# Kernel optimization log

Measured on AMD Instinct MI355X. Metric: run time of the kernel, lower is better.

## Reference

```python
import jax, jax.numpy as jnp
import numpy as np

DIM = 1024
NUM_HEADS = 16
HEAD_DIM = DIM // NUM_HEADS
B, L = 4, 4096


def setup_inputs() -> dict:
    key = jax.random.key(0)
    ks = jax.random.split(key, 11)
    s = 1.0 / np.sqrt(DIM)
    inp = {
        'q_seq': jax.random.normal(ks[0], (B, L, DIM), jnp.float32),
        'k_seq': jax.random.normal(ks[1], (B, L, DIM), jnp.float32),
        'v_seq': jax.random.normal(ks[2], (B, L, DIM), jnp.float32),
        'Wq': jax.random.normal(ks[3], (DIM, DIM), jnp.float32) * s,
        'bq': jax.random.normal(ks[4], (DIM,), jnp.float32) * s,
        'Wk': jax.random.normal(ks[5], (DIM, DIM), jnp.float32) * s,
        'bk': jax.random.normal(ks[6], (DIM,), jnp.float32) * s,
        'Wv': jax.random.normal(ks[7], (DIM, DIM), jnp.float32) * s,
        'bv': jax.random.normal(ks[8], (DIM,), jnp.float32) * s,
        'Wo': jax.random.normal(ks[9], (DIM, DIM), jnp.float32) * s,
        'bo': jax.random.normal(ks[10], (DIM,), jnp.float32) * s,
        'extract_common': 1,
    }
    return inp


def _heads(x):
    # [B, L, DIM] -> [B, H, L, D]
    Bb, Ll, _ = x.shape
    return x.reshape(Bb, Ll, NUM_HEADS, HEAD_DIM).transpose(0, 2, 1, 3)


def reference(q_seq, k_seq, v_seq, Wq, bq, Wk, bk, Wv, bv, Wo, bo, extract_common):
    Q = _heads(q_seq @ Wq.T + bq)   # [B, H, Lq, D]
    K = _heads(k_seq @ Wk.T + bk)   # [B, H, Lk, D]
    V = _heads(v_seq @ Wv.T + bv)   # [B, H, Lv, D]
    # softmax over the sequence dimension of K (torch dim=2 of [B,H,L,D])
    K_probs = jax.nn.softmax(K, axis=2)
    # context = K_probs^T @ V : [B, H, D, D]
    context = jnp.einsum('bhld,bhle->bhde', K_probs, V)
    attended = jnp.einsum('bhld,bhde->bhle', Q, context)  # [B, H, Lq, D]
    if extract_common:
        target = attended
    else:
        target = V - attended
    Bb, _, Ll, _ = target.shape
    target = target.transpose(0, 2, 1, 3).reshape(Bb, Ll, DIM)
    return target @ Wo.T + bo
```

## Files before the change

kernel.cpp:

```cpp
#include <hip/hip_runtime.h>
#include <cmath>

typedef __bf16 bf16x8 __attribute__((ext_vector_type(8)));
typedef float f32x4 __attribute__((ext_vector_type(4)));
typedef unsigned short us8 __attribute__((ext_vector_type(8)));

__device__ __forceinline__ unsigned short f2bf(float f) {
    union { float f; unsigned u; } x; x.f = f;
    unsigned u = x.u + 0x7FFFu + ((x.u >> 16) & 1u);
    return (unsigned short)(u >> 16);
}
__device__ __forceinline__ float bf2f(unsigned short h) {
    union { unsigned u; float f; } x; x.u = ((unsigned)h) << 16;
    return x.f;
}

__device__ __forceinline__ us8 cvt8(const float* p) {
    f32x4 a = *(const f32x4*)p;
    f32x4 b = *(const f32x4*)(p + 4);
    union { bf16x8 h; us8 u; } cv;
    cv.h[0] = (__bf16)a[0]; cv.h[1] = (__bf16)a[1];
    cv.h[2] = (__bf16)a[2]; cv.h[3] = (__bf16)a[3];
    cv.h[4] = (__bf16)b[0]; cv.h[5] = (__bf16)b[1];
    cv.h[6] = (__bf16)b[2]; cv.h[7] = (__bf16)b[3];
    return cv.u;
}

__device__ __forceinline__ void gl2lds16(const unsigned short* g, unsigned short* l) {
    __builtin_amdgcn_global_load_lds(
        (const __attribute__((address_space(1))) unsigned int*)g,
        (__attribute__((address_space(3))) unsigned int*)l, 16, 0, 0);
}

__global__ __launch_bounds__(256)
void cvt_kernel(const float* __restrict__ src, unsigned short* __restrict__ dst) {
    const size_t i = ((size_t)blockIdx.x * 256 + threadIdx.x) * 8;
    *(us8*)(dst + i) = cvt8(src + i);
}

__global__ __launch_bounds__(256)
void cvt_w4(const float* __restrict__ s0, const float* __restrict__ s1,
            const float* __restrict__ s2, const float* __restrict__ s3,
            unsigned short* __restrict__ d0, unsigned short* __restrict__ d1,
            unsigned short* __restrict__ d2, unsigned short* __restrict__ d3) {
    const float* sp[4] = {s0, s1, s2, s3};
    unsigned short* dp[4] = {d0, d1, d2, d3};
    const float* src = sp[blockIdx.y];
    unsigned short* dst = dp[blockIdx.y];
    const size_t i = ((size_t)blockIdx.x * 256 + threadIdx.x) * 8;
    *(us8*)(dst + i) = cvt8(src + i);
}

__device__ __forceinline__ void swz_tiles(int& m0, int& n0) {
    const int slot = blockIdx.x + (blockIdx.y << 3);
    const int w = ((slot & 7) << 7) | (slot >> 3);
    m0 = (w >> 3) << 7;
    n0 = (w & 7) << 7;
}

template<int MODE, bool BF>
__global__ __launch_bounds__(256)
void gemm_proj(const void* __restrict__ Ap, const void* __restrict__ Wp,
               const float* __restrict__ bias,
               unsigned short* __restrict__ outT,
               float* __restrict__ S)
{
    __shared__ __align__(16) unsigned short lds[17408];

    const int tid = threadIdx.x;
    const int wid = tid >> 6, lane = tid & 63;
    const int quad = lane >> 4, l16 = lane & 15;
    const int waveM = wid >> 1, waveN = wid & 1;
    int m0, n0; swz_tiles(m0, n0);
    const int srow = tid >> 2;
    const int scol = (tid & 3) * 8;
    const int r4 = lane >> 2, c8 = (lane & 3) * 8;

    f32x4 acc[4][4] = {};

    if (BF) {
        const unsigned short* A = (const unsigned short*)Ap;
        const unsigned short* W = (const unsigned short*)Wp;
        for (int s = wid; s < 8; s += 4) {
            const int row = s * 16 + r4;
            gl2lds16(A + (size_t)(m0 + row) * 1024 + c8, lds + s * 512);
            gl2lds16(W + (size_t)(n0 + row) * 1024 + c8, lds + 4096 + s * 512);
        }
    } else {
        const float* A = (const float*)Ap;
        const float* W = (const float*)Wp;
#pragma unroll
        for (int p = 0; p < 2; ++p) {
            const int row = p * 64 + srow;
            *(us8*)(lds + row * 32 + scol) = cvt8(A + (size_t)(m0 + row) * 1024 + scol);
            *(us8*)(lds + 4096 + row * 32 + scol) = cvt8(W + (size_t)(n0 + row) * 1024 + scol);
        }
    }
    __syncthreads();

    int cur = 0;
    for (int k0 = 0; k0 < 1024; k0 += 32) {
        const int nxt = cur ^ 1;
        if (k0 < 992) {
            if (BF) {
                const unsigned short* A = (const unsigned short*)Ap;
                const unsigned short* W = (const unsigned short*)Wp;
                for (int s = wid; s < 8; s += 4) {
                    const int row = s * 16 + r4;
                    gl2lds16(A + (size_t)(m0 + row) * 1024 + k0 + 32 + c8,
                             lds + nxt * 8192 + s * 512);
                    gl2lds16(W + (size_t)(n0 + row) * 1024 + k0 + 32 + c8,
                             lds + nxt * 8192 + 4096 + s * 512);
                }
            } else {
                const float* A = (const float*)Ap;
                const float* W = (const float*)Wp;
#pragma unroll
                for (int p = 0; p < 2; ++p) {
                    const int row = p * 64 + srow;
                    *(us8*)(lds + nxt * 8192 + row * 32 + scol) =
                        cvt8(A + (size_t)(m0 + row) * 1024 + k0 + 32 + scol);
                    *(us8*)(lds + nxt * 8192 + 4096 + row * 32 + scol) =
                        cvt8(W + (size_t)(n0 + row) * 1024 + k0 + 32 + scol);
                }
            }
        }
        const unsigned short* ldsA = lds + cur * 8192;
        const unsigned short* ldsB = ldsA + 4096;
        bf16x8 af[4], bfr[4];
#pragma unroll
        for (int i = 0; i < 4; ++i)
            af[i] = *(const bf16x8*)(ldsA + (waveM * 64 + i * 16 + l16) * 32 + quad * 8);
#pragma unroll
        for (int j = 0; j < 4; ++j)
            bfr[j] = *(const bf16x8*)(ldsB + (waveN * 64 + j * 16 + l16) * 32 + quad * 8);
#pragma unroll
        for (int i = 0; i < 4; ++i)
#pragma unroll
            for (int j = 0; j < 4; ++j)
                acc[i][j] = __builtin_amdgcn_mfma_f32_16x16x32_bf16(af[i], bfr[j], acc[i][j], 0, 0, 0);
        __syncthreads();
        cur = nxt;
    }

    const int b = m0 >> 12, l0 = m0 & 4095;
#pragma unroll
    for (int j = 0; j < 4; ++j) {
        const int nn = waveN * 64 + j * 16 + l16;
        const float bc = bias[n0 + nn];
        float ssum = 0.f;
#pragma unroll
        for (int i = 0; i < 4; ++i)
#pragma unroll
            for (int r = 0; r < 4; ++r) {
                const int mm = waveM * 64 + i * 16 + quad * 4 + r;
                float v = acc[i][j][r] + bc;
                if (MODE == 1) v = expf(fminf(fmaxf(v, -30.f), 30.f));
                lds[nn * 136 + mm] = f2bf(v);
                ssum += v;
            }
        if (MODE == 1) {
            ssum += __shfl_xor(ssum, 16);
            ssum += __shfl_xor(ssum, 32);
            if (lane < 16)
                atomicAdd(&S[(size_t)b * 1024 + n0 + waveN * 64 + j * 16 + lane], ssum);
        }
    }
    __syncthreads();
    const int seg = (tid & 15) * 8;
#pragma unroll
    for (int it = 0; it < 8; ++it) {
        const int nn = (tid >> 4) + it * 16;
        us8 v = *(const us8*)&lds[nn * 136 + seg];
        *(us8*)(outT + ((size_t)b * 1024 + n0 + nn) * 4096 + l0 + seg) = v;
    }
}

__global__ __launch_bounds__(256)
void ctx_kernel(const unsigned short* __restrict__ Vt,
                const unsigned short* __restrict__ Et,
                float* __restrict__ ctxf)
{
    __shared__ __align__(16) unsigned short lds[8192];

    const int tid = threadIdx.x;
    const int wid = tid >> 6, lane = tid & 63;
    const int quad = lane >> 4, l16 = lane & 15;
    const int b = blockIdx.z, h = blockIdx.y;
    const int lbase = blockIdx.x * 512;

    const unsigned short* Arow = Vt + ((size_t)b * 1024 + h * 64) * 4096;
    const unsigned short* Brow = Et + ((size_t)b * 1024 + h * 64) * 4096;

    const int srow = tid >> 2;
    const int scol = (tid & 3) * 8;

    f32x4 acc[4] = {};

    {
        us8 va = *(const us8*)(Arow + (size_t)srow * 4096 + lbase + scol);
        us8 vb = *(const us8*)(Brow + (size_t)srow * 4096 + lbase + scol);
        *(us8*)(lds + srow * 32 + scol) = va;
        *(us8*)(lds + 2048 + srow * 32 + scol) = vb;
    }
    __syncthreads();

    int cur = 0;
    for (int k0 = 0; k0 < 512; k0 += 32) {
        const int nxt = cur ^ 1;
        us8 na = {}, nb = {};
        const bool pf = (k0 < 480);
        if (pf) {
            na = *(const us8*)(Arow + (size_t)srow * 4096 + lbase + k0 + 32 + scol);
            nb = *(const us8*)(Brow + (size_t)srow * 4096 + lbase + k0 + 32 + scol);
        }
        const unsigned short* ldsA = lds + cur * 4096;
        const unsigned short* ldsB = ldsA + 2048;
        bf16x8 a = *(const bf16x8*)(ldsA + (wid * 16 + l16) * 32 + quad * 8);
#pragma unroll
        for (int j = 0; j < 4; ++j) {
            bf16x8 bb = *(const bf16x8*)(ldsB + (j * 16 + l16) * 32 + quad * 8);
            acc[j] = __builtin_amdgcn_mfma_f32_16x16x32_bf16(a, bb, acc[j], 0, 0, 0);
        }
        if (pf) {
            *(us8*)(lds + nxt * 4096 + srow * 32 + scol) = na;
            *(us8*)(lds + nxt * 4096 + 2048 + srow * 32 + scol) = nb;
        }
        __syncthreads();
        cur = nxt;
    }
    float* base = ctxf + ((size_t)(b * 16 + h)) * 4096;
#pragma unroll
    for (int j = 0; j < 4; ++j)
#pragma unroll
        for (int r = 0; r < 4; ++r) {
            const int e = wid * 16 + quad * 4 + r;
            const int d = j * 16 + l16;
            atomicAdd(base + e * 64 + d, acc[j][r]);
        }
}

__global__ __launch_bounds__(256)
void ctx_norm(const float* __restrict__ ctxf, const float* __restrict__ S,
              unsigned short* __restrict__ ctxb)
{
    const int i = blockIdx.x * 256 + threadIdx.x;
    const int d = i & 63;
    const int bh = i >> 12;
    const int b = bh >> 4, h = bh & 15;
    ctxb[i] = f2bf(ctxf[i] / S[b * 1024 + h * 64 + d]);
}

template<bool BF>
__global__ __launch_bounds__(256)
void gemm_qattn(const void* __restrict__ Ap, const void* __restrict__ Wp,
                const float* __restrict__ bias,
                const unsigned short* __restrict__ ctxb,
                const unsigned short* __restrict__ Vt,
                const int* __restrict__ ec,
                unsigned short* __restrict__ att)
{
    __shared__ __align__(16) unsigned short lds[26624];
    unsigned short* ldsQ = lds;
    unsigned short* ldsC = lds + 17408;

    const int tid = threadIdx.x;
    const int wid = tid >> 6, lane = tid & 63;
    const int quad = lane >> 4, l16 = lane & 15;
    const int waveM = wid >> 1, waveN = wid & 1;
    int m0, n0; swz_tiles(m0, n0);
    const int b = m0 >> 12;
    const int srow = tid >> 2, scol = (tid & 3) * 8;
    const int r4 = lane >> 2, c8 = (lane & 3) * 8;

    {
        const int e2 = tid >> 1;
        const int sg = (tid & 1) * 32;
        const unsigned short* src = ctxb +
            (((size_t)(b * 16) + (n0 >> 6) + (e2 >> 6)) * 64 + (e2 & 63)) * 64 + sg;
#pragma unroll
        for (int u = 0; u < 4; ++u)
            *(us8*)&ldsC[e2 * 72 + sg + u * 8] = *(const us8*)(src + u * 8);
    }

    f32x4 acc[4][4] = {};

    if (BF) {
        const unsigned short* A = (const unsigned short*)Ap;
        const unsigned short* W = (const unsigned short*)Wp;
        for (int s = wid; s < 8; s += 4) {
            const int row = s * 16 + r4;
            gl2lds16(A + (size_t)(m0 + row) * 1024 + c8, lds + s * 512);
            gl2lds16(W + (size_t)(n0 + row) * 1024 + c8, lds + 4096 + s * 512);
        }
    } else {
        const float* A = (const float*)Ap;
        const float* W = (const float*)Wp;
#pragma unroll
        for (int p = 0; p < 2; ++p) {
            const int row = p * 64 + srow;
            *(us8*)(lds + row * 32 + scol) = cvt8(A + (size_t)(m0 + row) * 1024 + scol);
            *(us8*)(lds + 4096 + row * 32 + scol) = cvt8(W + (size_t)(n0 + row) * 1024 + scol);
        }
    }
    __syncthreads();

    int cur = 0;
    for (int k0 = 0; k0 < 1024; k0 += 32) {
        const int nxt = cur ^ 1;
        if (k0 < 992) {
            if (BF) {
                const unsigned short* A = (const unsigned short*)Ap;
                const unsigned short* W = (const unsigned short*)Wp;
                for (int s = wid; s < 8; s += 4) {
                    const int row = s * 16 + r4;
                    gl2lds16(A + (size_t)(m0 + row) * 1024 + k0 + 32 + c8,
                             lds + nxt * 8192 + s * 512);
                    gl2lds16(W + (size_t)(n0 + row) * 1024 + k0 + 32 + c8,
                             lds + nxt * 8192 + 4096 + s * 512);
                }
            } else {
                const float* A = (const float*)Ap;
                const float* W = (const float*)Wp;
#pragma unroll
                for (int p = 0; p < 2; ++p) {
                    const int row = p * 64 + srow;
                    *(us8*)(lds + nxt * 8192 + row * 32 + scol) =
                        cvt8(A + (size_t)(m0 + row) * 1024 + k0 + 32 + scol);
                    *(us8*)(lds + nxt * 8192 + 4096 + row * 32 + scol) =
                        cvt8(W + (size_t)(n0 + row) * 1024 + k0 + 32 + scol);
                }
            }
        }
        const unsigned short* ldsA = lds + cur * 8192;
        const unsigned short* ldsB = ldsA + 4096;
        bf16x8 af[4], bfr[4];
#pragma unroll
        for (int i = 0; i < 4; ++i)
            af[i] = *(const bf16x8*)(ldsA + (waveM * 64 + i * 16 + l16) * 32 + quad * 8);
#pragma unroll
        for (int j = 0; j < 4; ++j)
            bfr[j] = *(const bf16x8*)(ldsB + (waveN * 64 + j * 16 + l16) * 32 + quad * 8);
#pragma unroll
        for (int i = 0; i < 4; ++i)
#pragma unroll
            for (int j = 0; j < 4; ++j)
                acc[i][j] = __builtin_amdgcn_mfma_f32_16x16x32_bf16(af[i], bfr[j], acc[i][j], 0, 0, 0);
        __syncthreads();
        cur = nxt;
    }

#pragma unroll
    for (int j = 0; j < 4; ++j) {
        const int nn = waveN * 64 + j * 16 + l16;
        const float bc = bias[n0 + nn];
#pragma unroll
        for (int i = 0; i < 4; ++i)
#pragma unroll
            for (int r = 0; r < 4; ++r) {
                const int mm = waveM * 64 + i * 16 + quad * 4 + r;
                ldsQ[mm * 136 + nn] = f2bf(acc[i][j][r] + bc);
            }
    }
    __syncthreads();

    f32x4 acc2[4][4] = {};
#pragma unroll
    for (int ks = 0; ks < 64; ks += 32) {
        bf16x8 aq[4], cq[4];
#pragma unroll
        for (int i = 0; i < 4; ++i)
            aq[i] = *(const bf16x8*)&ldsQ[(waveM * 64 + i * 16 + l16) * 136 + waveN * 64 + ks + quad * 8];
#pragma unroll
        for (int j = 0; j < 4; ++j)
            cq[j] = *(const bf16x8*)&ldsC[(waveN * 64 + j * 16 + l16) * 72 + ks + quad * 8];
#pragma unroll
        for (int i = 0; i < 4; ++i)
#pragma unroll
            for (int j = 0; j < 4; ++j)
                acc2[i][j] = __builtin_amdgcn_mfma_f32_16x16x32_bf16(aq[i], cq[j], acc2[i][j], 0, 0, 0);
    }

    const int common = ec[0];
#pragma unroll
    for (int i = 0; i < 4; ++i)
#pragma unroll
        for (int j = 0; j < 4; ++j)
#pragma unroll
            for (int r = 0; r < 4; ++r) {
                const int lrow = m0 + waveM * 64 + i * 16 + quad * 4 + r;
                const int chan = n0 + waveN * 64 + j * 16 + l16;
                float vv = acc2[i][j][r];
                if (!common)
                    vv = bf2f(Vt[((size_t)(lrow >> 12) * 1024 + chan) * 4096 + (lrow & 4095)]) - vv;
                att[(size_t)lrow * 1024 + chan] = f2bf(vv);
            }
}

template<bool BF>
__global__ __launch_bounds__(256)
void gemm_out(const unsigned short* __restrict__ A, const void* __restrict__ Wp,
              const float* __restrict__ bias,
              float* __restrict__ outP)
{
    __shared__ __align__(16) unsigned short lds[16384];

    const int tid = threadIdx.x;
    const int wid = tid >> 6, lane = tid & 63;
    const int quad = lane >> 4, l16 = lane & 15;
    const int waveM = wid >> 1, waveN = wid & 1;
    int m0, n0; swz_tiles(m0, n0);
    const int srow = tid >> 2, scol = (tid & 3) * 8;
    const int r4 = lane >> 2, c8 = (lane & 3) * 8;

    f32x4 acc[4][4] = {};

    if (BF) {
        const unsigned short* W = (const unsigned short*)Wp;
        for (int s = wid; s < 8; s += 4) {
            const int row = s * 16 + r4;
            gl2lds16(A + (size_t)(m0 + row) * 1024 + c8, lds + s * 512);
            gl2lds16(W + (size_t)(n0 + row) * 1024 + c8, lds + 4096 + s * 512);
        }
    } else {
        const float* W = (const float*)Wp;
#pragma unroll
        for (int p = 0; p < 2; ++p) {
            const int row = p * 64 + srow;
            *(us8*)(lds + row * 32 + scol) = *(const us8*)(A + (size_t)(m0 + row) * 1024 + scol);
            *(us8*)(lds + 4096 + row * 32 + scol) = cvt8(W + (size_t)(n0 + row) * 1024 + scol);
        }
    }
    __syncthreads();

    int cur = 0;
    for (int k0 = 0; k0 < 1024; k0 += 32) {
        const int nxt = cur ^ 1;
        if (k0 < 992) {
            if (BF) {
                const unsigned short* W = (const unsigned short*)Wp;
                for (int s = wid; s < 8; s += 4) {
                    const int row = s * 16 + r4;
                    gl2lds16(A + (size_t)(m0 + row) * 1024 + k0 + 32 + c8,
                             lds + nxt * 8192 + s * 512);
                    gl2lds16(W + (size_t)(n0 + row) * 1024 + k0 + 32 + c8,
                             lds + nxt * 8192 + 4096 + s * 512);
                }
            } else {
                const float* W = (const float*)Wp;
#pragma unroll
                for (int p = 0; p < 2; ++p) {
                    const int row = p * 64 + srow;
                    *(us8*)(lds + nxt * 8192 + row * 32 + scol) =
                        *(const us8*)(A + (size_t)(m0 + row) * 1024 + k0 + 32 + scol);
                    *(us8*)(lds + nxt * 8192 + 4096 + row * 32 + scol) =
                        cvt8(W + (size_t)(n0 + row) * 1024 + k0 + 32 + scol);
                }
            }
        }
        const unsigned short* ldsA = lds + cur * 8192;
        const unsigned short* ldsB = ldsA + 4096;
        bf16x8 af[4], bfr[4];
#pragma unroll
        for (int i = 0; i < 4; ++i)
            af[i] = *(const bf16x8*)(ldsA + (waveM * 64 + i * 16 + l16) * 32 + quad * 8);
#pragma unroll
        for (int j = 0; j < 4; ++j)
            bfr[j] = *(const bf16x8*)(ldsB + (waveN * 64 + j * 16 + l16) * 32 + quad * 8);
#pragma unroll
        for (int i = 0; i < 4; ++i)
#pragma unroll
            for (int j = 0; j < 4; ++j)
                acc[i][j] = __builtin_amdgcn_mfma_f32_16x16x32_bf16(af[i], bfr[j], acc[i][j], 0, 0, 0);
        __syncthreads();
        cur = nxt;
    }

#pragma unroll
    for (int j = 0; j < 4; ++j) {
        const int col = n0 + waveN * 64 + j * 16 + l16;
        const float bc = bias[col];
#pragma unroll
        for (int i = 0; i < 4; ++i)
#pragma unroll
            for (int r = 0; r < 4; ++r) {
                const int row = m0 + waveM * 64 + i * 16 + quad * 4 + r;
                outP[(size_t)row * 1024 + col] = acc[i][j][r] + bc;
            }
    }
}

extern "C" void kernel_launch(void* const* d_in, const int* in_sizes, int n_in,
                              void* d_out, int out_size, void* d_ws, size_t ws_size,
                              hipStream_t stream)
{
    const float* q  = (const float*)d_in[0];
    const float* k  = (const float*)d_in[1];
    const float* v  = (const float*)d_in[2];
    const float* Wq = (const float*)d_in[3];
    const float* bq = (const float*)d_in[4];
    const float* Wk = (const float*)d_in[5];
    const float* bk = (const float*)d_in[6];
    const float* Wv = (const float*)d_in[7];
    const float* bv = (const float*)d_in[8];
    const float* Wo = (const float*)d_in[9];
    const float* bo = (const float*)d_in[10];
    const int* ec   = (const int*)d_in[11];

    char* ws = (char*)d_ws;
    const size_t NEED_FAST = 110641152;
    const dim3 gblk(8, 128, 1);
    const dim3 gctx(8, 16, 4);

    if (ws_size >= NEED_FAST) {
        unsigned short* Ab   = (unsigned short*)(ws);
        unsigned short* Et   = (unsigned short*)(ws + 33554432);
        unsigned short* Vt   = (unsigned short*)(ws + 67108864);
        unsigned short* Wkb  = (unsigned short*)(ws + 100663296);
        unsigned short* Wvb  = (unsigned short*)(ws + 102760448);
        unsigned short* Wqb  = (unsigned short*)(ws + 104857600);
        unsigned short* Wob  = (unsigned short*)(ws + 106954752);
        float*          ctxf = (float*)(ws + 109051904);
        float*          S    = (float*)(ws + 110100480);
        unsigned short* ctxb = (unsigned short*)(ws + 110116864);
        unsigned short* att  = Et;

        hipMemsetAsync(S, 0, 4096 * sizeof(float), stream);
        hipMemsetAsync(ctxf, 0, 4 * 16 * 64 * 64 * sizeof(float), stream);

        cvt_w4<<<dim3(512, 4), 256, 0, stream>>>(Wk, Wv, Wq, Wo, Wkb, Wvb, Wqb, Wob);

        cvt_kernel<<<8192, 256, 0, stream>>>(k, Ab);
        gemm_proj<1, true><<<gblk, 256, 0, stream>>>(Ab, Wkb, bk, Et, S);

        cvt_kernel<<<8192, 256, 0, stream>>>(v, Ab);
        gemm_proj<2, true><<<gblk, 256, 0, stream>>>(Ab, Wvb, bv, Vt, nullptr);

        ctx_kernel<<<gctx, 256, 0, stream>>>(Vt, Et, ctxf);
        ctx_norm<<<1024, 256, 0, stream>>>(ctxf, S, ctxb);

        cvt_kernel<<<8192, 256, 0, stream>>>(q, Ab);
        gemm_qattn<true><<<gblk, 256, 0, stream>>>(Ab, Wqb, bq, ctxb, Vt, ec, att);

        gemm_out<true><<<gblk, 256, 0, stream>>>(att, Wob, bo, (float*)d_out);
    } else {
        unsigned short* Et   = (unsigned short*)(ws);
        unsigned short* Vt   = (unsigned short*)(ws + 33554432);
        float*          ctxf = (float*)(ws + 67108864);
        float*          S    = (float*)(ws + 68157440);
        unsigned short* ctxb = (unsigned short*)(ws + 68173824);
        unsigned short* att  = Et;

        hipMemsetAsync(S, 0, 4096 * sizeof(float), stream);
        hipMemsetAsync(ctxf, 0, 4 * 16 * 64 * 64 * sizeof(float), stream);

        gemm_proj<1, false><<<gblk, 256, 0, stream>>>(k, Wk, bk, Et, S);
        gemm_proj<2, false><<<gblk, 256, 0, stream>>>(v, Wv, bv, Vt, nullptr);
        ctx_kernel<<<gctx, 256, 0, stream>>>(Vt, Et, ctxf);
        ctx_norm<<<1024, 256, 0, stream>>>(ctxf, S, ctxb);
        gemm_qattn<false><<<gblk, 256, 0, stream>>>(q, Wq, bq, ctxb, Vt, ec, att);
        gemm_out<false><<<gblk, 256, 0, stream>>>(att, Wo, bo, (float*)d_out);
    }
}
```

Measured before the change: 458.3 us.

## Fuse activation fp32-to-bf16 conversion and context normalization into GEMM kernels

Drops the three standalone cvt_kernel passes over q/k/v and the ctx_norm kernel. The projection GEMMs now read fp32 activations directly. They prefetch the next K tile into registers before the MFMAs and pack to bf16 into LDS after them. The qattn kernel divides ctxf by S while loading its context tile. This removes a full write and re-read of three 32MB bf16 buffers plus several launches. In exchange, the GEMMs read twice the activation bytes per tile and hold more registers, and the async LDS load path for A is lost.

```diff
diff --git a/kernel.cpp b/kernel.cpp
--- a/kernel.cpp
+++ b/kernel.cpp
@@ -15,9 +15,7 @@
     return x.f;
 }
 
-__device__ __forceinline__ us8 cvt8(const float* p) {
-    f32x4 a = *(const f32x4*)p;
-    f32x4 b = *(const f32x4*)(p + 4);
+__device__ __forceinline__ us8 pack8(f32x4 a, f32x4 b) {
     union { bf16x8 h; us8 u; } cv;
     cv.h[0] = (__bf16)a[0]; cv.h[1] = (__bf16)a[1];
     cv.h[2] = (__bf16)a[2]; cv.h[3] = (__bf16)a[3];
@@ -26,16 +24,16 @@
     return cv.u;
 }
 
+__device__ __forceinline__ us8 cvt8(const float* p) {
+    f32x4 a = *(const f32x4*)p;
+    f32x4 b = *(const f32x4*)(p + 4);
+    return pack8(a, b);
+}
+
 __device__ __forceinline__ void gl2lds16(const unsigned short* g, unsigned short* l) {
     __builtin_amdgcn_global_load_lds(
         (const __attribute__((address_space(1))) unsigned int*)g,
         (__attribute__((address_space(3))) unsigned int*)l, 16, 0, 0);
-}
-
-__global__ __launch_bounds__(256)
-void cvt_kernel(const float* __restrict__ src, unsigned short* __restrict__ dst) {
-    const size_t i = ((size_t)blockIdx.x * 256 + threadIdx.x) * 8;
-    *(us8*)(dst + i) = cvt8(src + i);
 }
 
 __global__ __launch_bounds__(256)
@@ -58,9 +56,9 @@
     n0 = (w & 7) << 7;
 }
 
-template<int MODE, bool BF>
+template<int MODE, bool WBF>
 __global__ __launch_bounds__(256)
-void gemm_proj(const void* __restrict__ Ap, const void* __restrict__ Wp,
+void gemm_proj(const float* __restrict__ A, const void* __restrict__ Wp,
                const float* __restrict__ bias,
                unsigned short* __restrict__ outT,
                float* __restrict__ S)
@@ -72,56 +70,52 @@
     const int quad = lane >> 4, l16 = lane & 15;
     const int waveM = wid >> 1, waveN = wid & 1;
     int m0, n0; swz_tiles(m0, n0);
-    const int srow = tid >> 2;
-    const int scol = (tid & 3) * 8;
+    const int srow = tid >> 2, scol = (tid & 3) * 8;
     const int r4 = lane >> 2, c8 = (lane & 3) * 8;
 
     f32x4 acc[4][4] = {};
 
-    if (BF) {
-        const unsigned short* A = (const unsigned short*)Ap;
+    if (WBF) {
         const unsigned short* W = (const unsigned short*)Wp;
-        for (int s = wid; s < 8; s += 4) {
-            const int row = s * 16 + r4;
-            gl2lds16(A + (size_t)(m0 + row) * 1024 + c8, lds + s * 512);
-            gl2lds16(W + (size_t)(n0 + row) * 1024 + c8, lds + 4096 + s * 512);
-        }
+        for (int s = wid; s < 8; s += 4)
+            gl2lds16(W + (size_t)(n0 + s * 16 + r4) * 1024 + c8, lds + 4096 + s * 512);
     } else {
-        const float* A = (const float*)Ap;
         const float* W = (const float*)Wp;
 #pragma unroll
-        for (int p = 0; p < 2; ++p) {
-            const int row = p * 64 + srow;
-            *(us8*)(lds + row * 32 + scol) = cvt8(A + (size_t)(m0 + row) * 1024 + scol);
-            *(us8*)(lds + 4096 + row * 32 + scol) = cvt8(W + (size_t)(n0 + row) * 1024 + scol);
-        }
-    }
+        for (int p = 0; p < 2; ++p)
+            *(us8*)(lds + 4096 + (p * 64 + srow) * 32 + scol) =
+                cvt8(W + (size_t)(n0 + p * 64 + srow) * 1024 + scol);
+    }
+#pragma unroll
+    for (int p = 0; p < 2; ++p)
+        *(us8*)(lds + (p * 64 + srow) * 32 + scol) =
+            cvt8(A + (size_t)(m0 + p * 64 + srow) * 1024 + scol);
     __syncthreads();
 
     int cur = 0;
     for (int k0 = 0; k0 < 1024; k0 += 32) {
         const int nxt = cur ^ 1;
-        if (k0 < 992) {
-            if (BF) {
-                const unsigned short* A = (const unsigned short*)Ap;
+        const bool pf = (k0 < 992);
+        f32x4 pa[2][2], pw[2][2];
+        if (pf) {
+#pragma unroll
+            for (int p = 0; p < 2; ++p) {
+                const float* src = A + (size_t)(m0 + p * 64 + srow) * 1024 + k0 + 32 + scol;
+                pa[p][0] = *(const f32x4*)src;
+                pa[p][1] = *(const f32x4*)(src + 4);
+            }
+            if (WBF) {
                 const unsigned short* W = (const unsigned short*)Wp;
-                for (int s = wid; s < 8; s += 4) {
-                    const int row = s * 16 + r4;
-                    gl2lds16(A + (size_t)(m0 + row) * 1024 + k0 + 32 + c8,
-                             lds + nxt * 8192 + s * 512);
-                    gl2lds16(W + (size_t)(n0 + row) * 1024 + k0 + 32 + c8,
+                for (int s = wid; s < 8; s += 4)
+                    gl2lds16(W + (size_t)(n0 + s * 16 + r4) * 1024 + k0 + 32 + c8,
                              lds + nxt * 8192 + 4096 + s * 512);
-                }
             } else {
-                const float* A = (const float*)Ap;
                 const float* W = (const float*)Wp;
 #pragma unroll
                 for (int p = 0; p < 2; ++p) {
-                    const int row = p * 64 + srow;
-                    *(us8*)(lds + nxt * 8192 + row * 32 + scol) =
-                        cvt8(A + (size_t)(m0 + row) * 1024 + k0 + 32 + scol);
-                    *(us8*)(lds + nxt * 8192 + 4096 + row * 32 + scol) =
-                        cvt8(W + (size_t)(n0 + row) * 1024 + k0 + 32 + scol);
+                    const float* srcw = W + (size_t)(n0 + p * 64 + srow) * 1024 + k0 + 32 + scol;
+                    pw[p][0] = *(const f32x4*)srcw;
+                    pw[p][1] = *(const f32x4*)(srcw + 4);
                 }
             }
         }
@@ -139,6 +133,16 @@
 #pragma unroll
             for (int j = 0; j < 4; ++j)
                 acc[i][j] = __builtin_amdgcn_mfma_f32_16x16x32_bf16(af[i], bfr[j], acc[i][j], 0, 0, 0);
+        if (pf) {
+#pragma unroll
+            for (int p = 0; p < 2; ++p)
+                *(us8*)(lds + nxt * 8192 + (p * 64 + srow) * 32 + scol) = pack8(pa[p][0], pa[p][1]);
+            if (!WBF) {
+#pragma unroll
+                for (int p = 0; p < 2; ++p)
+                    *(us8*)(lds + nxt * 8192 + 4096 + (p * 64 + srow) * 32 + scol) = pack8(pw[p][0], pw[p][1]);
+            }
+        }
         __syncthreads();
         cur = nxt;
     }
@@ -240,22 +244,12 @@
         }
 }
 
+template<bool WBF>
 __global__ __launch_bounds__(256)
-void ctx_norm(const float* __restrict__ ctxf, const float* __restrict__ S,
-              unsigned short* __restrict__ ctxb)
-{
-    const int i = blockIdx.x * 256 + threadIdx.x;
-    const int d = i & 63;
-    const int bh = i >> 12;
-    const int b = bh >> 4, h = bh & 15;
-    ctxb[i] = f2bf(ctxf[i] / S[b * 1024 + h * 64 + d]);
-}
-
-template<bool BF>
-__global__ __launch_bounds__(256)
-void gemm_qattn(const void* __restrict__ Ap, const void* __restrict__ Wp,
+void gemm_qattn(const float* __restrict__ A, const void* __restrict__ Wp,
                 const float* __restrict__ bias,
-                const unsigned short* __restrict__ ctxb,
+                const float* __restrict__ ctxf,
+                const float* __restrict__ Sv,
                 const unsigned short* __restrict__ Vt,
                 const int* __restrict__ ec,
                 unsigned short* __restrict__ att)
@@ -276,59 +270,65 @@
     {
         const int e2 = tid >> 1;
         const int sg = (tid & 1) * 32;
-        const unsigned short* src = ctxb +
-            (((size_t)(b * 16) + (n0 >> 6) + (e2 >> 6)) * 64 + (e2 & 63)) * 64 + sg;
-#pragma unroll
-        for (int u = 0; u < 4; ++u)
-            *(us8*)&ldsC[e2 * 72 + sg + u * 8] = *(const us8*)(src + u * 8);
+        const int hh = (n0 >> 6) + (e2 >> 6);
+        const float* srcf = ctxf + (((size_t)(b * 16) + hh) * 64 + (e2 & 63)) * 64 + sg;
+        const float* Sp = Sv + (size_t)b * 1024 + hh * 64 + sg;
+#pragma unroll
+        for (int u = 0; u < 4; ++u) {
+            f32x4 c0 = *(const f32x4*)(srcf + u * 8);
+            f32x4 c1 = *(const f32x4*)(srcf + u * 8 + 4);
+            union { bf16x8 h; us8 uu; } cv;
+#pragma unroll
+            for (int j = 0; j < 4; ++j) cv.h[j] = (__bf16)(c0[j] / Sp[u * 8 + j]);
+#pragma unroll
+            for (int j = 0; j < 4; ++j) cv.h[4 + j] = (__bf16)(c1[j] / Sp[u * 8 + 4 + j]);
+            *(us8*)&ldsC[e2 * 72 + sg + u * 8] = cv.uu;
+        }
     }
 
     f32x4 acc[4][4] = {};
 
-    if (BF) {
-        const unsigned short* A = (const unsigned short*)Ap;
+    if (WBF) {
         const unsigned short* W = (const unsigned short*)Wp;
-        for (int s = wid; s < 8; s += 4) {
-            const int row = s * 16 + r4;
-            gl2lds16(A + (size_t)(m0 + row) * 1024 + c8, lds + s * 512);
-            gl2lds16(W + (size_t)(n0 + row) * 1024 + c8, lds + 4096 + s * 512);
-        }
+        for (int s = wid; s < 8; s += 4)
+            gl2lds16(W + (size_t)(n0 + s * 16 + r4) * 1024 + c8, lds + 4096 + s * 512);
     } else {
-        const float* A = (const float*)Ap;
         const float* W = (const float*)Wp;
 #pragma unroll
-        for (int p = 0; p < 2; ++p) {
-            const int row = p * 64 + srow;
-            *(us8*)(lds + row * 32 + scol) = cvt8(A + (size_t)(m0 + row) * 1024 + scol);
-            *(us8*)(lds + 4096 + row * 32 + scol) = cvt8(W + (size_t)(n0 + row) * 1024 + scol);
-        }
-    }
+        for (int p = 0; p < 2; ++p)
+            *(us8*)(lds + 4096 + (p * 64 + srow) * 32 + scol) =
+                cvt8(W + (size_t)(n0 + p * 64 + srow) * 1024 + scol);
+    }
+#pragma unroll
+    for (int p = 0; p < 2; ++p)
+        *(us8*)(lds + (p * 64 + srow) * 32 + scol) =
+            cvt8(A + (size_t)(m0 + p * 64 + srow) * 1024 + scol);
     __syncthreads();
 
     int cur = 0;
     for (int k0 = 0; k0 < 1024; k0 += 32) {
         const int nxt = cur ^ 1;
-        if (k0 < 992) {
-            if (BF) {
-                const unsigned short* A = (const unsigned short*)Ap;
+        const bool pf = (k0 < 992);
+        f32x4 pa[2][2], pw[2][2];
+        if (pf) {
+#pragma unroll
+            for (int p = 0; p < 2; ++p) {
+                const float* src = A + (size_t)(m0 + p * 64 + srow) * 1024 + k0 + 32 + scol;
+                pa[p][0] = *(const f32x4*)src;
+                pa[p][1] = *(const f32x4*)(src + 4);
+            }
+            if (WBF) {
                 const unsigned short* W = (const unsigned short*)Wp;
-                for (int s = wid; s < 8; s += 4) {
-                    const int row = s * 16 + r4;
-                    gl2lds16(A + (size_t)(m0 + row) * 1024 + k0 + 32 + c8,
-                             lds + nxt * 8192 + s * 512);
-                    gl2lds16(W + (size_t)(n0 + row) * 1024 + k0 + 32 + c8,
+                for (int s = wid; s < 8; s += 4)
+                    gl2lds16(W + (size_t)(n0 + s * 16 + r4) * 1024 + k0 + 32 + c8,
                              lds + nxt * 8192 + 4096 + s * 512);
-                }
             } else {
-                const float* A = (const float*)Ap;
                 const float* W = (const float*)Wp;
 #pragma unroll
                 for (int p = 0; p < 2; ++p) {
-                    const int row = p * 64 + srow;
-                    *(us8*)(lds + nxt * 8192 + row * 32 + scol) =
-                        cvt8(A + (size_t)(m0 + row) * 1024 + k0 + 32 + scol);
-                    *(us8*)(lds + nxt * 8192 + 4096 + row * 32 + scol) =
-                        cvt8(W + (size_t)(n0 + row) * 1024 + k0 + 32 + scol);
+                    const float* srcw = W + (size_t)(n0 + p * 64 + srow) * 1024 + k0 + 32 + scol;
+                    pw[p][0] = *(const f32x4*)srcw;
+                    pw[p][1] = *(const f32x4*)(srcw + 4);
                 }
             }
         }
@@ -346,6 +346,16 @@
 #pragma unroll
             for (int j = 0; j < 4; ++j)
                 acc[i][j] = __builtin_amdgcn_mfma_f32_16x16x32_bf16(af[i], bfr[j], acc[i][j], 0, 0, 0);
+        if (pf) {
+#pragma unroll
+            for (int p = 0; p < 2; ++p)
+                *(us8*)(lds + nxt * 8192 + (p * 64 + srow) * 32 + scol) = pack8(pa[p][0], pa[p][1]);
+            if (!WBF) {
+#pragma unroll
+                for (int p = 0; p < 2; ++p)
+                    *(us8*)(lds + nxt * 8192 + 4096 + (p * 64 + srow) * 32 + scol) = pack8(pw[p][0], pw[p][1]);
+            }
+        }
         __syncthreads();
         cur = nxt;
     }
@@ -397,7 +407,7 @@
             }
 }
 
-template<bool BF>
+template<bool WBF>
 __global__ __launch_bounds__(256)
 void gemm_out(const unsigned short* __restrict__ A, const void* __restrict__ Wp,
               const float* __restrict__ bias,
@@ -415,7 +425,7 @@
 
     f32x4 acc[4][4] = {};
 
-    if (BF) {
+    if (WBF) {
         const unsigned short* W = (const unsigned short*)Wp;
         for (int s = wid; s < 8; s += 4) {
             const int row = s * 16 + r4;
@@ -437,7 +447,7 @@
     for (int k0 = 0; k0 < 1024; k0 += 32) {
         const int nxt = cur ^ 1;
         if (k0 < 992) {
-            if (BF) {
+            if (WBF) {
                 const unsigned short* W = (const unsigned short*)Wp;
                 for (int s = wid; s < 8; s += 4) {
                     const int row = s * 16 + r4;
@@ -508,21 +518,19 @@
     const int* ec   = (const int*)d_in[11];
 
     char* ws = (char*)d_ws;
-    const size_t NEED_FAST = 110641152;
+    const size_t NEED_FAST = 76562432;
     const dim3 gblk(8, 128, 1);
     const dim3 gctx(8, 16, 4);
 
     if (ws_size >= NEED_FAST) {
-        unsigned short* Ab   = (unsigned short*)(ws);
-        unsigned short* Et   = (unsigned short*)(ws + 33554432);
-        unsigned short* Vt   = (unsigned short*)(ws + 67108864);
-        unsigned short* Wkb  = (unsigned short*)(ws + 100663296);
-        unsigned short* Wvb  = (unsigned short*)(ws + 102760448);
-        unsigned short* Wqb  = (unsigned short*)(ws + 104857600);
-        unsigned short* Wob  = (unsigned short*)(ws + 106954752);
-        float*          ctxf = (float*)(ws + 109051904);
-        float*          S    = (float*)(ws + 110100480);
-        unsigned short* ctxb = (unsigned short*)(ws + 110116864);
+        unsigned short* Et   = (unsigned short*)(ws);
+        unsigned short* Vt   = (unsigned short*)(ws + 33554432);
+        unsigned short* Wkb  = (unsigned short*)(ws + 67108864);
+        unsigned short* Wvb  = (unsigned short*)(ws + 69206016);
+        unsigned short* Wqb  = (unsigned short*)(ws + 71303168);
+        unsigned short* Wob  = (unsigned short*)(ws + 73400320);
+        float*          ctxf = (float*)(ws + 75497472);
+        float*          S    = (float*)(ws + 76546048);
         unsigned short* att  = Et;
 
         hipMemsetAsync(S, 0, 4096 * sizeof(float), stream);
@@ -530,17 +538,12 @@
 
         cvt_w4<<<dim3(512, 4), 256, 0, stream>>>(Wk, Wv, Wq, Wo, Wkb, Wvb, Wqb, Wob);
 
-        cvt_kernel<<<8192, 256, 0, stream>>>(k, Ab);
-        gemm_proj<1, true><<<gblk, 256, 0, stream>>>(Ab, Wkb, bk, Et, S);
-
-        cvt_kernel<<<8192, 256, 0, stream>>>(v, Ab);
-        gemm_proj<2, true><<<gblk, 256, 0, stream>>>(Ab, Wvb, bv, Vt, nullptr);
+        gemm_proj<1, true><<<gblk, 256, 0, stream>>>(k, Wkb, bk, Et, S);
+        gemm_proj<2, true><<<gblk, 256, 0, stream>>>(v, Wvb, bv, Vt, nullptr);
 
         ctx_kernel<<<gctx, 256, 0, stream>>>(Vt, Et, ctxf);
-        ctx_norm<<<1024, 256, 0, stream>>>(ctxf, S, ctxb);
-
-        cvt_kernel<<<8192, 256, 0, stream>>>(q, Ab);
-        gemm_qattn<true><<<gblk, 256, 0, stream>>>(Ab, Wqb, bq, ctxb, Vt, ec, att);
+
+        gemm_qattn<true><<<gblk, 256, 0, stream>>>(q, Wqb, bq, ctxf, S, Vt, ec, att);
 
         gemm_out<true><<<gblk, 256, 0, stream>>>(att, Wob, bo, (float*)d_out);
     } else {
@@ -548,7 +551,6 @@
         unsigned short* Vt   = (unsigned short*)(ws + 33554432);
         float*          ctxf = (float*)(ws + 67108864);
         float*          S    = (float*)(ws + 68157440);
-        unsigned short* ctxb = (unsigned short*)(ws + 68173824);
         unsigned short* att  = Et;
 
         hipMemsetAsync(S, 0, 4096 * sizeof(float), stream);
@@ -557,8 +559,7 @@
         gemm_proj<1, false><<<gblk, 256, 0, stream>>>(k, Wk, bk, Et, S);
         gemm_proj<2, false><<<gblk, 256, 0, stream>>>(v, Wv, bv, Vt, nullptr);
         ctx_kernel<<<gctx, 256, 0, stream>>>(Vt, Et, ctxf);
-        ctx_norm<<<1024, 256, 0, stream>>>(ctxf, S, ctxb);
-        gemm_qattn<false><<<gblk, 256, 0, stream>>>(q, Wq, bq, ctxb, Vt, ec, att);
+        gemm_qattn<false><<<gblk, 256, 0, stream>>>(q, Wq, bq, ctxf, S, Vt, ec, att);
         gemm_out<false><<<gblk, 256, 0, stream>>>(att, Wo, bo, (float*)d_out);
     }
 }
```

Result: slower. 512.4 us (+11.8%).
